# Optimization experiments

Hardware: AMD Instinct MI355X
Metric: run time of the kernel (lower is better)

Reference implementation:

```python
import jax, jax.numpy as jnp
import numpy as np

N_HEAD = 16


def setup_inputs() -> dict:
    key = jax.random.key(0)
    ks = jax.random.split(key, 7)
    b, lq, lv = 2, 2048, 2048
    q_dim = k_dim = v_dim = 1024
    s = 0.02
    return {
        "q": jax.random.normal(ks[0], (b, lq, q_dim), jnp.float32),
        "k": jax.random.normal(ks[1], (b, lv, k_dim), jnp.float32),
        "v": jax.random.normal(ks[2], (b, lv, v_dim), jnp.float32),
        "Wq": jax.random.normal(ks[3], (k_dim, q_dim), jnp.float32) * s,  # torch Linear: [out, in]
        "Wk": jax.random.normal(ks[4], (k_dim, k_dim), jnp.float32) * s,
        "Wv": jax.random.normal(ks[5], (v_dim, v_dim), jnp.float32) * s,
        "Wo": jax.random.normal(ks[6], (v_dim, v_dim), jnp.float32) * s,
    }


def reference(q, k, v, Wq, Wk, Wv, Wo):
    b, lq, _ = q.shape
    lv = k.shape[1]
    qp = q @ Wq.T  # [b, lq, k_dim]
    kp = k @ Wk.T  # [b, lv, k_dim]
    vp = v @ Wv.T  # [b, lv, v_dim]
    # split heads: [b, h, l, d]
    qh = qp.reshape(b, lq, N_HEAD, -1).transpose(0, 2, 1, 3)
    kh = kp.reshape(b, lv, N_HEAD, -1).transpose(0, 2, 1, 3)
    vh = vp.reshape(b, lv, N_HEAD, -1).transpose(0, 2, 1, 3)
    d = qh.shape[-1]
    scores = jnp.einsum("bhqd,bhkd->bhqk", qh, kh) / jnp.sqrt(jnp.float32(d))
    p = jax.nn.softmax(scores, axis=-1)
    attn = jnp.einsum("bhqk,bhkd->bhqd", p, vh)
    attn = attn.transpose(0, 2, 1, 3).reshape(b, lq, -1)  # [b, lq, v_dim]
    return attn @ Wo.T
```

## Files before the change

kernel.cpp:

```cpp
#include <hip/hip_runtime.h>
#include <hip/hip_bf16.h>
#include <stdint.h>

typedef __attribute__((ext_vector_type(8))) short bf16x8;
typedef __attribute__((ext_vector_type(4))) float f32x4;
typedef __attribute__((ext_vector_type(16))) float f32x16;
typedef __attribute__((ext_vector_type(2))) uint32_t u32x2;
typedef __attribute__((ext_vector_type(4))) uint32_t u32x4;

#define LQ 2048
#define CDIM 1024
#define NTOK 4096
#define WELEM 1048576
#define TELEM 4194304

__device__ __forceinline__ short f2bf(float f) {
  union { float f; uint32_t u; } v; v.f = f;
  uint32_t r = v.u + 0x7fffu + ((v.u >> 16) & 1u);
  return (short)(r >> 16);
}

__device__ __forceinline__ uint32_t cvt_pk_bf16(float a, float b) {
  uint32_t r;
  asm("v_cvt_pk_bf16_f32 %0, %1, %2" : "=v"(r) : "v"(a), "v"(b));
  return r;
}

__device__ __forceinline__ float fexp2(float x) {
  float r;
  asm("v_exp_f32 %0, %1" : "=v"(r) : "v"(x));
  return r;
}

__device__ __forceinline__ int swz(int row, int col) {
  return (row << 6) + (col ^ ((row & 7) << 3));
}

__device__ __forceinline__ void gl_lds16(const void* g, void* lds) {
  __builtin_amdgcn_global_load_lds(
      (const __attribute__((address_space(1))) void*)g,
      (__attribute__((address_space(3))) void*)lds, 16, 0, 0);
}

__device__ __forceinline__ void plswap(uint32_t& a, uint32_t& b) {
  asm volatile("s_nop 1\n\tv_permlane32_swap_b32 %0, %1\n\ts_nop 1" : "+v"(a), "+v"(b));
}

__device__ __forceinline__ bf16x8 mkfrag(const float* p) {
  uint32_t w0 = cvt_pk_bf16(p[0], p[1]);
  uint32_t w1 = cvt_pk_bf16(p[2], p[3]);
  uint32_t w2 = cvt_pk_bf16(p[4], p[5]);
  uint32_t w3 = cvt_pk_bf16(p[6], p[7]);
  plswap(w0, w2);
  plswap(w1, w3);
  union { u32x4 u; bf16x8 h; } cv;
  cv.u = u32x4{w0, w1, w2, w3};
  return cv.h;
}

__global__ __launch_bounds__(256) void convall_kernel(const float* __restrict__ wq, const float* __restrict__ wk,
                                                      const float* __restrict__ wv, const float* __restrict__ wo,
                                                      const float* __restrict__ q, const float* __restrict__ k,
                                                      const float* __restrict__ v,
                                                      short* __restrict__ wbf, short* __restrict__ qb,
                                                      short* __restrict__ kb, short* __restrict__ vb) {
  const int NG = (4 * WELEM + 3 * TELEM) / 8;
  for (int i = blockIdx.x * 256 + threadIdx.x; i < NG; i += gridDim.x * 256) {
    int e = i * 8;
    const float* s;
    short* d;
    if (e < 4 * WELEM) {
      int seg = e >> 20;
      int off = e & (WELEM - 1);
      s = (seg == 0 ? wq : seg == 1 ? wk : seg == 2 ? wv : wo) + off;
      d = wbf + e;
    } else {
      int j = e - 4 * WELEM;
      int which = j >> 22;
      int off = j & (TELEM - 1);
      s = (which == 0 ? q : which == 1 ? k : v) + off;
      d = (which == 0 ? qb : which == 1 ? kb : vb) + off;
    }
    f32x4 x0 = *(const f32x4*)(s);
    f32x4 x1 = *(const f32x4*)(s + 4);
    u32x4 r = { cvt_pk_bf16(x0[0], x0[1]), cvt_pk_bf16(x0[2], x0[3]),
                cvt_pk_bf16(x1[0], x1[1]), cvt_pk_bf16(x1[2], x1[3]) };
    *(u32x4*)(d) = r;
  }
}

template<int CMODE, int BN>
__device__ __forceinline__ void gemm_bb(short* __restrict__ AbP, short* __restrict__ BbP,
                                        const short* __restrict__ Ap, const short* __restrict__ Bp,
                                        void* Cp, int m0, int n0, int K, int ldc)
{
  const int t = threadIdx.x;
  const int lane = t & 63;
  const int wid = t >> 6;
  const int l15 = lane & 15, l4 = lane >> 4;
  constexpr int NI = (BN == 128) ? 4 : 2;
  const int wr = (BN == 128) ? (wid >> 1) * 64 : wid * 32;
  const int wc = (BN == 128) ? (wid & 1) * 64 : 0;

  f32x4 acc[NI][4];
#pragma unroll
  for (int i = 0; i < NI; ++i)
#pragma unroll
    for (int j = 0; j < 4; ++j) acc[i][j] = f32x4{0.f, 0.f, 0.f, 0.f};

  const int grow = lane >> 3;
  const int gcol = ((lane & 7) ^ grow) * 8;
  constexpr int AI = 4, BI = BN / 32;
  const short* asrc = Ap + (size_t)(m0 + wid * 32 + grow) * K + gcol;
  const short* bsrc = Bp + (size_t)(n0 + wid * (BN / 4) + grow) * K + gcol;

#pragma unroll
  for (int c = 0; c < AI; ++c) gl_lds16(asrc + (size_t)c * 8 * K, AbP + (wid * AI + c) * 512);
#pragma unroll
  for (int c = 0; c < BI; ++c) gl_lds16(bsrc + (size_t)c * 8 * K, BbP + (wid * BI + c) * 512);

  const int NT = K / 64;
  for (int kt = 0; kt < NT; ++kt) {
    const int cur = kt & 1;
    if (kt + 1 < NT) {
      const short* a2 = asrc + (size_t)(kt + 1) * 64;
      const short* b2 = bsrc + (size_t)(kt + 1) * 64;
#pragma unroll
      for (int c = 0; c < AI; ++c)
        gl_lds16(a2 + (size_t)c * 8 * K, AbP + (cur ^ 1) * 8192 + (wid * AI + c) * 512);
#pragma unroll
      for (int c = 0; c < BI; ++c)
        gl_lds16(b2 + (size_t)c * 8 * K, BbP + (cur ^ 1) * (BN * 64) + (wid * BI + c) * 512);
      if constexpr (BN == 128) asm volatile("s_waitcnt vmcnt(8)" ::: "memory");
      else                     asm volatile("s_waitcnt vmcnt(6)" ::: "memory");
    } else {
      asm volatile("s_waitcnt vmcnt(0)" ::: "memory");
    }
    __builtin_amdgcn_sched_barrier(0);
    __builtin_amdgcn_s_barrier();
    __builtin_amdgcn_sched_barrier(0);

    const short* Al = AbP + cur * 8192;
    const short* Bl = BbP + cur * (BN * 64);
#pragma unroll
    for (int kh = 0; kh < 2; ++kh) {
      bf16x8 af[NI], bfr[4];
#pragma unroll
      for (int i = 0; i < NI; ++i)
        af[i] = *(const bf16x8*)&Al[swz(wr + i * 16 + l15, kh * 32 + l4 * 8)];
#pragma unroll
      for (int j = 0; j < 4; ++j)
        bfr[j] = *(const bf16x8*)&Bl[swz(wc + j * 16 + l15, kh * 32 + l4 * 8)];
      __builtin_amdgcn_s_setprio(1);
#pragma unroll
      for (int i = 0; i < NI; ++i)
#pragma unroll
        for (int j = 0; j < 4; ++j)
          acc[i][j] = __builtin_amdgcn_mfma_f32_16x16x32_bf16(af[i], bfr[j], acc[i][j], 0, 0, 0);
      __builtin_amdgcn_s_setprio(0);
    }
    __builtin_amdgcn_sched_barrier(0);
    __builtin_amdgcn_s_barrier();
  }

#pragma unroll
  for (int i = 0; i < NI; ++i)
#pragma unroll
    for (int j = 0; j < 4; ++j) {
      if constexpr (CMODE == 2) {
        int rr0 = m0 + wr + i * 16 + l4 * 4;
        int cc = n0 + wc + j * 16 + l15;
        size_t idx = ((size_t)(((rr0 >> 11) << 4) + (cc >> 6)) * 64 + (cc & 63)) * 2048 + (rr0 & 2047);
        u32x2 w = { cvt_pk_bf16(acc[i][j][0], acc[i][j][1]),
                    cvt_pk_bf16(acc[i][j][2], acc[i][j][3]) };
        *(u32x2*)((short*)Cp + idx) = w;
      } else {
#pragma unroll
        for (int r = 0; r < 4; ++r) {
          int rr = m0 + wr + i * 16 + l4 * 4 + r;
          int cc = n0 + wc + j * 16 + l15;
          if constexpr (CMODE == 0) ((float*)Cp)[(size_t)rr * ldc + cc] = acc[i][j][r];
          else                      ((short*)Cp)[(size_t)rr * ldc + cc] = f2bf(acc[i][j][r]);
        }
      }
    }
}

__global__ __launch_bounds__(256) void proj_kernel(const short* __restrict__ qb, const short* __restrict__ kb,
                                                   const short* __restrict__ vb, const short* __restrict__ wbf,
                                                   short* __restrict__ qp, short* __restrict__ kp,
                                                   short* __restrict__ vpt)
{
  __shared__ alignas(16) short Ab[2 * 8192];
  __shared__ alignas(16) short Bb[2 * 8192];
  int nb = blockIdx.y;
  int sel = nb >> 3;
  int n0 = (nb & 7) * 128;
  int m0 = blockIdx.x * 128;
  if (sel == 2) {
    gemm_bb<2, 128>(Ab, Bb, vb, wbf + (size_t)2 * WELEM, vpt, m0, n0, CDIM, CDIM);
  } else {
    const short* A = sel == 0 ? qb : kb;
    const short* B = wbf + (size_t)sel * WELEM;
    short* C = sel == 0 ? qp : kp;
    gemm_bb<1, 128>(Ab, Bb, A, B, C, m0, n0, CDIM, CDIM);
  }
}

__global__ __launch_bounds__(256) void out_kernel(const short* __restrict__ at, const short* __restrict__ wo,
                                                  float* __restrict__ out)
{
  __shared__ alignas(16) short Ab[2 * 8192];
  __shared__ alignas(16) short Bb[2 * 4096];
  gemm_bb<0, 64>(Ab, Bb, at, wo, out, blockIdx.x * 128, blockIdx.y * 64, CDIM, CDIM);
}

__global__ __launch_bounds__(256) void attn_kernel(const short* __restrict__ kp, const short* __restrict__ vpt,
                                                   short* __restrict__ qp)
{
  __shared__ alignas(16) short Kbuf[2][64 * 64];
  __shared__ alignas(16) short Vbuf[2][64 * 64];

  const int bh = blockIdx.x;
  const int b = bh >> 4, h = bh & 15;
  const int q0 = blockIdx.y * 128;
  const int t = threadIdx.x, lane = t & 63, wid = t >> 6;
  const int l31 = lane & 31, hi = lane >> 5;
  const size_t base = (size_t)b * LQ * CDIM + (size_t)h * 64;
  const int qw = q0 + wid * 32;

  bf16x8 qf[4];
  {
    const short* qrow = qp + base + (size_t)(qw + l31) * CDIM + hi * 8;
    qf[0] = *(const bf16x8*)(qrow);
    qf[1] = *(const bf16x8*)(qrow + 16);
    qf[2] = *(const bf16x8*)(qrow + 32);
    qf[3] = *(const bf16x8*)(qrow + 48);
  }

  bf16x8 ones;
#pragma unroll
  for (int j = 0; j < 8; ++j) ones[j] = (short)0x3F80;

  f32x16 o0, o1, lacc;
#pragma unroll
  for (int r = 0; r < 16; ++r) { o0[r] = 0.f; o1[r] = 0.f; lacc[r] = 0.f; }

  const int grp = lane >> 3;
  const int chk = ((lane & 7) ^ grp) * 8;
  const short* ksrc = kp + base + (size_t)(wid * 16 + grp) * CDIM + chk;
  const short* vsrc = vpt + (size_t)bh * 64 * 2048 + (size_t)(wid * 16 + grp) * 2048 + chk;

  const float SC2 = 0.18033688011112042f;
  const int NT = LQ / 64;

  gl_lds16(ksrc, &Kbuf[0][(wid * 16) * 64]);
  gl_lds16(ksrc + (size_t)8 * CDIM, &Kbuf[0][(wid * 16 + 8) * 64]);
  gl_lds16(vsrc, &Vbuf[0][(wid * 16) * 64]);
  gl_lds16(vsrc + (size_t)8 * 2048, &Vbuf[0][(wid * 16 + 8) * 64]);

  for (int kt = 0; kt < NT; ++kt) {
    const int cur = kt & 1;
    if (kt + 1 < NT) {
      const short* ks = ksrc + (size_t)(kt + 1) * 64 * CDIM;
      const short* vs = vsrc + (size_t)(kt + 1) * 64;
      gl_lds16(ks, &Kbuf[cur ^ 1][(wid * 16) * 64]);
      gl_lds16(ks + (size_t)8 * CDIM, &Kbuf[cur ^ 1][(wid * 16 + 8) * 64]);
      gl_lds16(vs, &Vbuf[cur ^ 1][(wid * 16) * 64]);
      gl_lds16(vs + (size_t)8 * 2048, &Vbuf[cur ^ 1][(wid * 16 + 8) * 64]);
      asm volatile("s_waitcnt vmcnt(4)" ::: "memory");
    } else {
      asm volatile("s_waitcnt vmcnt(0)" ::: "memory");
    }
    __builtin_amdgcn_sched_barrier(0);
    __builtin_amdgcn_s_barrier();
    __builtin_amdgcn_sched_barrier(0);

    const short* Klds = Kbuf[cur];
    const short* Vt = Vbuf[cur];

    f32x16 c0, c1;
#pragma unroll
    for (int r = 0; r < 16; ++r) { c0[r] = 0.f; c1[r] = 0.f; }
    __builtin_amdgcn_s_setprio(1);
#pragma unroll
    for (int ds = 0; ds < 4; ++ds) {
      bf16x8 ka = *(const bf16x8*)&Klds[swz(l31, ds * 16 + hi * 8)];
      bf16x8 kb = *(const bf16x8*)&Klds[swz(32 + l31, ds * 16 + hi * 8)];
      c0 = __builtin_amdgcn_mfma_f32_32x32x16_bf16(ka, qf[ds], c0, 0, 0, 0);
      c1 = __builtin_amdgcn_mfma_f32_32x32x16_bf16(kb, qf[ds], c1, 0, 0, 0);
    }
    __builtin_amdgcn_s_setprio(0);

    float pr0[16], pr1[16];
#pragma unroll
    for (int r = 0; r < 16; ++r) {
      pr0[r] = fexp2(c0[r] * SC2);
      pr1[r] = fexp2(c1[r] * SC2);
    }

    bf16x8 pa0 = mkfrag(pr0);
    bf16x8 pa1 = mkfrag(pr0 + 8);
    bf16x8 pa2 = mkfrag(pr1);
    bf16x8 pa3 = mkfrag(pr1 + 8);

    __builtin_amdgcn_s_setprio(1);
#pragma unroll
    for (int ks = 0; ks < 4; ++ks) {
      bf16x8 pa = ks == 0 ? pa0 : ks == 1 ? pa1 : ks == 2 ? pa2 : pa3;
      bf16x8 v0 = *(const bf16x8*)&Vt[swz(l31, ks * 16 + hi * 8)];
      bf16x8 v1 = *(const bf16x8*)&Vt[swz(32 + l31, ks * 16 + hi * 8)];
      o0 = __builtin_amdgcn_mfma_f32_32x32x16_bf16(v0, pa, o0, 0, 0, 0);
      o1 = __builtin_amdgcn_mfma_f32_32x32x16_bf16(v1, pa, o1, 0, 0, 0);
      lacc = __builtin_amdgcn_mfma_f32_32x32x16_bf16(ones, pa, lacc, 0, 0, 0);
    }
    __builtin_amdgcn_s_setprio(0);
    __builtin_amdgcn_sched_barrier(0);
    __builtin_amdgcn_s_barrier();
  }

  float inv = 1.0f / lacc[0];
  short* orow = qp + base + (size_t)(qw + l31) * CDIM;
#pragma unroll
  for (int rq = 0; rq < 4; ++rq) {
    u32x2 w;
    w[0] = cvt_pk_bf16(o0[rq * 4 + 0] * inv, o0[rq * 4 + 1] * inv);
    w[1] = cvt_pk_bf16(o0[rq * 4 + 2] * inv, o0[rq * 4 + 3] * inv);
    *(u32x2*)(orow + rq * 8 + hi * 4) = w;
    w[0] = cvt_pk_bf16(o1[rq * 4 + 0] * inv, o1[rq * 4 + 1] * inv);
    w[1] = cvt_pk_bf16(o1[rq * 4 + 2] * inv, o1[rq * 4 + 3] * inv);
    *(u32x2*)(orow + 32 + rq * 8 + hi * 4) = w;
  }
}

extern "C" void kernel_launch(void* const* d_in, const int* in_sizes, int n_in,
                              void* d_out, int out_size, void* d_ws, size_t ws_size,
                              hipStream_t stream) {
  const float* q  = (const float*)d_in[0];
  const float* k  = (const float*)d_in[1];
  const float* v  = (const float*)d_in[2];
  const float* Wq = (const float*)d_in[3];
  const float* Wk = (const float*)d_in[4];
  const float* Wv = (const float*)d_in[5];
  const float* Wo = (const float*)d_in[6];
  float* out = (float*)d_out;

  short* wbf = (short*)d_ws;
  short* vb  = wbf + (size_t)4 * WELEM;
  short* qp  = vb + (size_t)TELEM;
  short* kp  = qp + (size_t)TELEM;
  short* vpt = kp + (size_t)TELEM;
  short* qb = (short*)d_out;
  short* kb = qb + (size_t)TELEM;

  convall_kernel<<<2048, 256, 0, stream>>>(Wq, Wk, Wv, Wo, q, k, v, wbf, qb, kb, vb);
  proj_kernel<<<dim3(32, 24), 256, 0, stream>>>(qb, kb, vb, wbf, qp, kp, vpt);
  attn_kernel<<<dim3(32, 16), 256, 0, stream>>>(kp, vpt, qp);
  out_kernel<<<dim3(32, 16), 256, 0, stream>>>(qp, wbf + (size_t)3 * WELEM, out);
}
```

Measured before the change: 120.1 us.

## Fuse activation fp32-to-bf16 conversion into projection GEMM and split MFMA accumulators

After: 188.5 us. +56.9%, slower.

```diff
diff --git a/kernel.cpp b/kernel.cpp
--- a/kernel.cpp
+++ b/kernel.cpp
@@ -58,41 +58,27 @@
   return cv.h;
 }
 
-__global__ __launch_bounds__(256) void convall_kernel(const float* __restrict__ wq, const float* __restrict__ wk,
-                                                      const float* __restrict__ wv, const float* __restrict__ wo,
-                                                      const float* __restrict__ q, const float* __restrict__ k,
-                                                      const float* __restrict__ v,
-                                                      short* __restrict__ wbf, short* __restrict__ qb,
-                                                      short* __restrict__ kb, short* __restrict__ vb) {
-  const int NG = (4 * WELEM + 3 * TELEM) / 8;
+__global__ __launch_bounds__(256) void convw_kernel(const float* __restrict__ wq, const float* __restrict__ wk,
+                                                    const float* __restrict__ wv, const float* __restrict__ wo,
+                                                    short* __restrict__ wbf) {
+  const int NG = (4 * WELEM) / 8;
   for (int i = blockIdx.x * 256 + threadIdx.x; i < NG; i += gridDim.x * 256) {
     int e = i * 8;
-    const float* s;
-    short* d;
-    if (e < 4 * WELEM) {
-      int seg = e >> 20;
-      int off = e & (WELEM - 1);
-      s = (seg == 0 ? wq : seg == 1 ? wk : seg == 2 ? wv : wo) + off;
-      d = wbf + e;
-    } else {
-      int j = e - 4 * WELEM;
-      int which = j >> 22;
-      int off = j & (TELEM - 1);
-      s = (which == 0 ? q : which == 1 ? k : v) + off;
-      d = (which == 0 ? qb : which == 1 ? kb : vb) + off;
-    }
+    int seg = e >> 20;
+    int off = e & (WELEM - 1);
+    const float* s = (seg == 0 ? wq : seg == 1 ? wk : seg == 2 ? wv : wo) + off;
     f32x4 x0 = *(const f32x4*)(s);
     f32x4 x1 = *(const f32x4*)(s + 4);
     u32x4 r = { cvt_pk_bf16(x0[0], x0[1]), cvt_pk_bf16(x0[2], x0[3]),
                 cvt_pk_bf16(x1[0], x1[1]), cvt_pk_bf16(x1[2], x1[3]) };
-    *(u32x4*)(d) = r;
-  }
-}
-
-template<int CMODE, int BN>
+    *(u32x4*)(wbf + e) = r;
+  }
+}
+
+template<int CMODE, int BN, bool AF32>
 __device__ __forceinline__ void gemm_bb(short* __restrict__ AbP, short* __restrict__ BbP,
-                                        const short* __restrict__ Ap, const short* __restrict__ Bp,
-                                        void* Cp, int m0, int n0, int K, int ldc)
+                                        const void* Ap, const short* __restrict__ Bp,
+                                        void* Cp, int m0, int n0, int K, int ldc, float cscale)
 {
   const int t = threadIdx.x;
   const int lane = t & 63;
@@ -111,37 +97,72 @@
   const int grow = lane >> 3;
   const int gcol = ((lane & 7) ^ grow) * 8;
   constexpr int AI = 4, BI = BN / 32;
-  const short* asrc = Ap + (size_t)(m0 + wid * 32 + grow) * K + gcol;
   const short* bsrc = Bp + (size_t)(n0 + wid * (BN / 4) + grow) * K + gcol;
-
-#pragma unroll
-  for (int c = 0; c < AI; ++c) gl_lds16(asrc + (size_t)c * 8 * K, AbP + (wid * AI + c) * 512);
+  const short* asrcb = (const short*)Ap + (size_t)(m0 + wid * 32 + grow) * K + gcol;
+  const int arow = t >> 1, acol = (t & 1) * 32;
+  const float* asrcf = (const float*)Ap + (size_t)(m0 + arow) * K + acol;
+  f32x4 va[8];
+
 #pragma unroll
   for (int c = 0; c < BI; ++c) gl_lds16(bsrc + (size_t)c * 8 * K, BbP + (wid * BI + c) * 512);
+  if constexpr (AF32) {
+#pragma unroll
+    for (int c = 0; c < 8; ++c) va[c] = *(const f32x4*)(asrcf + c * 4);
+  } else {
+#pragma unroll
+    for (int c = 0; c < AI; ++c) gl_lds16(asrcb + (size_t)c * 8 * K, AbP + (wid * AI + c) * 512);
+  }
 
   const int NT = K / 64;
   for (int kt = 0; kt < NT; ++kt) {
     const int cur = kt & 1;
-    if (kt + 1 < NT) {
-      const short* a2 = asrc + (size_t)(kt + 1) * 64;
-      const short* b2 = bsrc + (size_t)(kt + 1) * 64;
-#pragma unroll
-      for (int c = 0; c < AI; ++c)
-        gl_lds16(a2 + (size_t)c * 8 * K, AbP + (cur ^ 1) * 8192 + (wid * AI + c) * 512);
-#pragma unroll
-      for (int c = 0; c < BI; ++c)
-        gl_lds16(b2 + (size_t)c * 8 * K, BbP + (cur ^ 1) * (BN * 64) + (wid * BI + c) * 512);
-      if constexpr (BN == 128) asm volatile("s_waitcnt vmcnt(8)" ::: "memory");
-      else                     asm volatile("s_waitcnt vmcnt(6)" ::: "memory");
+    short* Al = AbP + cur * 8192;
+    const short* Bl = BbP + cur * (BN * 64);
+
+    if constexpr (AF32) {
+      if (kt + 1 < NT) {
+        const short* b2 = bsrc + (size_t)(kt + 1) * 64;
+#pragma unroll
+        for (int c = 0; c < BI; ++c)
+          gl_lds16(b2 + (size_t)c * 8 * K, BbP + (cur ^ 1) * (BN * 64) + (wid * BI + c) * 512);
+        asm volatile("s_waitcnt vmcnt(4)" ::: "memory");
+      } else {
+        asm volatile("s_waitcnt vmcnt(0)" ::: "memory");
+      }
+#pragma unroll
+      for (int c2 = 0; c2 < 4; ++c2) {
+        u32x4 w = { cvt_pk_bf16(va[2 * c2][0], va[2 * c2][1]),
+                    cvt_pk_bf16(va[2 * c2][2], va[2 * c2][3]),
+                    cvt_pk_bf16(va[2 * c2 + 1][0], va[2 * c2 + 1][1]),
+                    cvt_pk_bf16(va[2 * c2 + 1][2], va[2 * c2 + 1][3]) };
+        *(u32x4*)&Al[swz(arow, acol + c2 * 8)] = w;
+      }
+      if (kt + 1 < NT) {
+        const float* a2 = asrcf + (size_t)(kt + 1) * 64;
+#pragma unroll
+        for (int c = 0; c < 8; ++c) va[c] = *(const f32x4*)(a2 + c * 4);
+      }
+      asm volatile("s_waitcnt lgkmcnt(0)" ::: "memory");
     } else {
-      asm volatile("s_waitcnt vmcnt(0)" ::: "memory");
+      if (kt + 1 < NT) {
+        const short* a2 = asrcb + (size_t)(kt + 1) * 64;
+        const short* b2 = bsrc + (size_t)(kt + 1) * 64;
+#pragma unroll
+        for (int c = 0; c < AI; ++c)
+          gl_lds16(a2 + (size_t)c * 8 * K, AbP + (cur ^ 1) * 8192 + (wid * AI + c) * 512);
+#pragma unroll
+        for (int c = 0; c < BI; ++c)
+          gl_lds16(b2 + (size_t)c * 8 * K, BbP + (cur ^ 1) * (BN * 64) + (wid * BI + c) * 512);
+        if constexpr (BN == 128) asm volatile("s_waitcnt vmcnt(8)" ::: "memory");
+        else                     asm volatile("s_waitcnt vmcnt(6)" ::: "memory");
+      } else {
+        asm volatile("s_waitcnt vmcnt(0)" ::: "memory");
+      }
     }
     __builtin_amdgcn_sched_barrier(0);
     __builtin_amdgcn_s_barrier();
     __builtin_amdgcn_sched_barrier(0);
 
-    const short* Al = AbP + cur * 8192;
-    const short* Bl = BbP + cur * (BN * 64);
 #pragma unroll
     for (int kh = 0; kh < 2; ++kh) {
       bf16x8 af[NI], bfr[4];
@@ -180,31 +201,30 @@
           int rr = m0 + wr + i * 16 + l4 * 4 + r;
           int cc = n0 + wc + j * 16 + l15;
           if constexpr (CMODE == 0) ((float*)Cp)[(size_t)rr * ldc + cc] = acc[i][j][r];
-          else                      ((short*)Cp)[(size_t)rr * ldc + cc] = f2bf(acc[i][j][r]);
+          else                      ((short*)Cp)[(size_t)rr * ldc + cc] = f2bf(acc[i][j][r] * cscale);
         }
       }
     }
 }
 
-__global__ __launch_bounds__(256) void proj_kernel(const short* __restrict__ qb, const short* __restrict__ kb,
-                                                   const short* __restrict__ vb, const short* __restrict__ wbf,
+__global__ __launch_bounds__(256) void proj_kernel(const float* __restrict__ q, const float* __restrict__ k,
+                                                   const float* __restrict__ v, const short* __restrict__ wbf,
                                                    short* __restrict__ qp, short* __restrict__ kp,
                                                    short* __restrict__ vpt)
 {
   __shared__ alignas(16) short Ab[2 * 8192];
   __shared__ alignas(16) short Bb[2 * 8192];
+  const float SC2 = 0.18033688011112042f;
   int nb = blockIdx.y;
   int sel = nb >> 3;
   int n0 = (nb & 7) * 128;
   int m0 = blockIdx.x * 128;
-  if (sel == 2) {
-    gemm_bb<2, 128>(Ab, Bb, vb, wbf + (size_t)2 * WELEM, vpt, m0, n0, CDIM, CDIM);
-  } else {
-    const short* A = sel == 0 ? qb : kb;
-    const short* B = wbf + (size_t)sel * WELEM;
-    short* C = sel == 0 ? qp : kp;
-    gemm_bb<1, 128>(Ab, Bb, A, B, C, m0, n0, CDIM, CDIM);
-  }
+  if (sel == 0)
+    gemm_bb<1, 128, true>(Ab, Bb, q, wbf, qp, m0, n0, CDIM, CDIM, SC2);
+  else if (sel == 1)
+    gemm_bb<1, 128, true>(Ab, Bb, k, wbf + (size_t)WELEM, kp, m0, n0, CDIM, CDIM, 1.0f);
+  else
+    gemm_bb<2, 128, true>(Ab, Bb, v, wbf + (size_t)2 * WELEM, vpt, m0, n0, CDIM, CDIM, 1.0f);
 }
 
 __global__ __launch_bounds__(256) void out_kernel(const short* __restrict__ at, const short* __restrict__ wo,
@@ -212,7 +232,7 @@
 {
   __shared__ alignas(16) short Ab[2 * 8192];
   __shared__ alignas(16) short Bb[2 * 4096];
-  gemm_bb<0, 64>(Ab, Bb, at, wo, out, blockIdx.x * 128, blockIdx.y * 64, CDIM, CDIM);
+  gemm_bb<0, 64, false>(Ab, Bb, at, wo, out, blockIdx.x * 128, blockIdx.y * 64, CDIM, CDIM, 1.0f);
 }
 
 __global__ __launch_bounds__(256) void attn_kernel(const short* __restrict__ kp, const short* __restrict__ vpt,
@@ -242,16 +262,17 @@
 #pragma unroll
   for (int j = 0; j < 8; ++j) ones[j] = (short)0x3F80;
 
-  f32x16 o0, o1, lacc;
-#pragma unroll
-  for (int r = 0; r < 16; ++r) { o0[r] = 0.f; o1[r] = 0.f; lacc[r] = 0.f; }
+  f32x16 o0a, o0b, o1a, o1b, lacca, laccb;
+#pragma unroll
+  for (int r = 0; r < 16; ++r) {
+    o0a[r] = 0.f; o0b[r] = 0.f; o1a[r] = 0.f; o1b[r] = 0.f; lacca[r] = 0.f; laccb[r] = 0.f;
+  }
 
   const int grp = lane >> 3;
   const int chk = ((lane & 7) ^ grp) * 8;
   const short* ksrc = kp + base + (size_t)(wid * 16 + grp) * CDIM + chk;
   const short* vsrc = vpt + (size_t)bh * 64 * 2048 + (size_t)(wid * 16 + grp) * 2048 + chk;
 
-  const float SC2 = 0.18033688011112042f;
   const int NT = LQ / 64;
 
   gl_lds16(ksrc, &Kbuf[0][(wid * 16) * 64]);
@@ -279,24 +300,29 @@
     const short* Klds = Kbuf[cur];
     const short* Vt = Vbuf[cur];
 
-    f32x16 c0, c1;
-#pragma unroll
-    for (int r = 0; r < 16; ++r) { c0[r] = 0.f; c1[r] = 0.f; }
+    f32x16 c0a, c0b, c1a, c1b;
+#pragma unroll
+    for (int r = 0; r < 16; ++r) { c0a[r] = 0.f; c0b[r] = 0.f; c1a[r] = 0.f; c1b[r] = 0.f; }
     __builtin_amdgcn_s_setprio(1);
 #pragma unroll
     for (int ds = 0; ds < 4; ++ds) {
       bf16x8 ka = *(const bf16x8*)&Klds[swz(l31, ds * 16 + hi * 8)];
       bf16x8 kb = *(const bf16x8*)&Klds[swz(32 + l31, ds * 16 + hi * 8)];
-      c0 = __builtin_amdgcn_mfma_f32_32x32x16_bf16(ka, qf[ds], c0, 0, 0, 0);
-      c1 = __builtin_amdgcn_mfma_f32_32x32x16_bf16(kb, qf[ds], c1, 0, 0, 0);
+      if (ds & 1) {
+        c0b = __builtin_amdgcn_mfma_f32_32x32x16_bf16(ka, qf[ds], c0b, 0, 0, 0);
+        c1b = __builtin_amdgcn_mfma_f32_32x32x16_bf16(kb, qf[ds], c1b, 0, 0, 0);
+      } else {
+        c0a = __builtin_amdgcn_mfma_f32_32x32x16_bf16(ka, qf[ds], c0a, 0, 0, 0);
+        c1a = __builtin_amdgcn_mfma_f32_32x32x16_bf16(kb, qf[ds], c1a, 0, 0, 0);
+      }
     }
     __builtin_amdgcn_s_setprio(0);
 
     float pr0[16], pr1[16];
 #pragma unroll
     for (int r = 0; r < 16; ++r) {
-      pr0[r] = fexp2(c0[r] * SC2);
-      pr1[r] = fexp2(c1[r] * SC2);
+      pr0[r] = fexp2(c0a[r] + c0b[r]);
+      pr1[r] = fexp2(c1a[r] + c1b[r]);
     }
 
     bf16x8 pa0 = mkfrag(pr0);
@@ -310,25 +336,35 @@
       bf16x8 pa = ks == 0 ? pa0 : ks == 1 ? pa1 : ks == 2 ? pa2 : pa3;
       bf16x8 v0 = *(const bf16x8*)&Vt[swz(l31, ks * 16 + hi * 8)];
       bf16x8 v1 = *(const bf16x8*)&Vt[swz(32 + l31, ks * 16 + hi * 8)];
-      o0 = __builtin_amdgcn_mfma_f32_32x32x16_bf16(v0, pa, o0, 0, 0, 0);
-      o1 = __builtin_amdgcn_mfma_f32_32x32x16_bf16(v1, pa, o1, 0, 0, 0);
-      lacc = __builtin_amdgcn_mfma_f32_32x32x16_bf16(ones, pa, lacc, 0, 0, 0);
+      if (ks < 2) {
+        o0a = __builtin_amdgcn_mfma_f32_32x32x16_bf16(v0, pa, o0a, 0, 0, 0);
+        o1a = __builtin_amdgcn_mfma_f32_32x32x16_bf16(v1, pa, o1a, 0, 0, 0);
+        lacca = __builtin_amdgcn_mfma_f32_32x32x16_bf16(ones, pa, lacca, 0, 0, 0);
+      } else {
+        o0b = __builtin_amdgcn_mfma_f32_32x32x16_bf16(v0, pa, o0b, 0, 0, 0);
+        o1b = __builtin_amdgcn_mfma_f32_32x32x16_bf16(v1, pa, o1b, 0, 0, 0);
+        laccb = __builtin_amdgcn_mfma_f32_32x32x16_bf16(ones, pa, laccb, 0, 0, 0);
+      }
     }
     __builtin_amdgcn_s_setprio(0);
     __builtin_amdgcn_sched_barrier(0);
     __builtin_amdgcn_s_barrier();
   }
 
-  float inv = 1.0f / lacc[0];
+  float inv = 1.0f / (lacca[0] + laccb[0]);
   short* orow = qp + base + (size_t)(qw + l31) * CDIM;
 #pragma unroll
   for (int rq = 0; rq < 4; ++rq) {
     u32x2 w;
-    w[0] = cvt_pk_bf16(o0[rq * 4 + 0] * inv, o0[rq * 4 + 1] * inv);
-    w[1] = cvt_pk_bf16(o0[rq * 4 + 2] * inv, o0[rq * 4 + 3] * inv);
+    w[0] = cvt_pk_bf16((o0a[rq * 4 + 0] + o0b[rq * 4 + 0]) * inv,
+                       (o0a[rq * 4 + 1] + o0b[rq * 4 + 1]) * inv);
+    w[1] = cvt_pk_bf16((o0a[rq * 4 + 2] + o0b[rq * 4 + 2]) * inv,
+                       (o0a[rq * 4 + 3] + o0b[rq * 4 + 3]) * inv);
     *(u32x2*)(orow + rq * 8 + hi * 4) = w;
-    w[0] = cvt_pk_bf16(o1[rq * 4 + 0] * inv, o1[rq * 4 + 1] * inv);
-    w[1] = cvt_pk_bf16(o1[rq * 4 + 2] * inv, o1[rq * 4 + 3] * inv);
+    w[0] = cvt_pk_bf16((o1a[rq * 4 + 0] + o1b[rq * 4 + 0]) * inv,
+                       (o1a[rq * 4 + 1] + o1b[rq * 4 + 1]) * inv);
+    w[1] = cvt_pk_bf16((o1a[rq * 4 + 2] + o1b[rq * 4 + 2]) * inv,
+                       (o1a[rq * 4 + 3] + o1b[rq * 4 + 3]) * inv);
     *(u32x2*)(orow + 32 + rq * 8 + hi * 4) = w;
   }
 }
@@ -346,15 +382,12 @@
   float* out = (float*)d_out;
 
   short* wbf = (short*)d_ws;
-  short* vb  = wbf + (size_t)4 * WELEM;
-  short* qp  = vb + (size_t)TELEM;
+  short* qp  = wbf + (size_t)4 * WELEM;
   short* kp  = qp + (size_t)TELEM;
   short* vpt = kp + (size_t)TELEM;
-  short* qb = (short*)d_out;
-  short* kb = qb + (size_t)TELEM;
-
-  convall_kernel<<<2048, 256, 0, stream>>>(Wq, Wk, Wv, Wo, q, k, v, wbf, qb, kb, vb);
-  proj_kernel<<<dim3(32, 24), 256, 0, stream>>>(qb, kb, vb, wbf, qp, kp, vpt);
+
+  convw_kernel<<<512, 256, 0, stream>>>(Wq, Wk, Wv, Wo, wbf);
+  proj_kernel<<<dim3(32, 24), 256, 0, stream>>>(q, k, v, wbf, qp, kp, vpt);
   attn_kernel<<<dim3(32, 16), 256, 0, stream>>>(kp, vpt, qp);
   out_kernel<<<dim3(32, 16), 256, 0, stream>>>(qp, wbf + (size_t)3 * WELEM, out);
 }
```

## Split attention over two KV halves and combine partial outputs in separate kernel

Applied to the files above, without the earlier changes.

New measurement: 128.2 us. +6.7%, slower.

```diff
diff --git a/kernel.cpp b/kernel.cpp
--- a/kernel.cpp
+++ b/kernel.cpp
@@ -18,6 +18,11 @@
   union { float f; uint32_t u; } v; v.f = f;
   uint32_t r = v.u + 0x7fffu + ((v.u >> 16) & 1u);
   return (short)(r >> 16);
+}
+
+__device__ __forceinline__ float bf2f(short s) {
+  union { uint32_t u; float f; } v; v.u = ((uint32_t)(uint16_t)s) << 16;
+  return v.f;
 }
 
 __device__ __forceinline__ uint32_t cvt_pk_bf16(float a, float b) {
@@ -92,7 +97,7 @@
 template<int CMODE, int BN>
 __device__ __forceinline__ void gemm_bb(short* __restrict__ AbP, short* __restrict__ BbP,
                                         const short* __restrict__ Ap, const short* __restrict__ Bp,
-                                        void* Cp, int m0, int n0, int K, int ldc)
+                                        void* Cp, int m0, int n0, int K, int ldc, float cscale)
 {
   const int t = threadIdx.x;
   const int lane = t & 63;
@@ -180,7 +185,7 @@
           int rr = m0 + wr + i * 16 + l4 * 4 + r;
           int cc = n0 + wc + j * 16 + l15;
           if constexpr (CMODE == 0) ((float*)Cp)[(size_t)rr * ldc + cc] = acc[i][j][r];
-          else                      ((short*)Cp)[(size_t)rr * ldc + cc] = f2bf(acc[i][j][r]);
+          else                      ((short*)Cp)[(size_t)rr * ldc + cc] = f2bf(acc[i][j][r] * cscale);
         }
       }
     }
@@ -193,18 +198,17 @@
 {
   __shared__ alignas(16) short Ab[2 * 8192];
   __shared__ alignas(16) short Bb[2 * 8192];
+  const float SC2 = 0.18033688011112042f;
   int nb = blockIdx.y;
   int sel = nb >> 3;
   int n0 = (nb & 7) * 128;
   int m0 = blockIdx.x * 128;
-  if (sel == 2) {
-    gemm_bb<2, 128>(Ab, Bb, vb, wbf + (size_t)2 * WELEM, vpt, m0, n0, CDIM, CDIM);
-  } else {
-    const short* A = sel == 0 ? qb : kb;
-    const short* B = wbf + (size_t)sel * WELEM;
-    short* C = sel == 0 ? qp : kp;
-    gemm_bb<1, 128>(Ab, Bb, A, B, C, m0, n0, CDIM, CDIM);
-  }
+  if (sel == 0)
+    gemm_bb<1, 128>(Ab, Bb, qb, wbf, qp, m0, n0, CDIM, CDIM, SC2);
+  else if (sel == 1)
+    gemm_bb<1, 128>(Ab, Bb, kb, wbf + (size_t)WELEM, kp, m0, n0, CDIM, CDIM, 1.0f);
+  else
+    gemm_bb<2, 128>(Ab, Bb, vb, wbf + (size_t)2 * WELEM, vpt, m0, n0, CDIM, CDIM, 1.0f);
 }
 
 __global__ __launch_bounds__(256) void out_kernel(const short* __restrict__ at, const short* __restrict__ wo,
@@ -212,11 +216,13 @@
 {
   __shared__ alignas(16) short Ab[2 * 8192];
   __shared__ alignas(16) short Bb[2 * 4096];
-  gemm_bb<0, 64>(Ab, Bb, at, wo, out, blockIdx.x * 128, blockIdx.y * 64, CDIM, CDIM);
+  gemm_bb<0, 64>(Ab, Bb, at, wo, out, blockIdx.x * 128, blockIdx.y * 64, CDIM, CDIM, 1.0f);
 }
 
 __global__ __launch_bounds__(256) void attn_kernel(const short* __restrict__ kp, const short* __restrict__ vpt,
-                                                   short* __restrict__ qp)
+                                                   const short* __restrict__ qp,
+                                                   short* __restrict__ op0, short* __restrict__ op1,
+                                                   float* __restrict__ laccbuf)
 {
   __shared__ alignas(16) short Kbuf[2][64 * 64];
   __shared__ alignas(16) short Vbuf[2][64 * 64];
@@ -224,6 +230,7 @@
   const int bh = blockIdx.x;
   const int b = bh >> 4, h = bh & 15;
   const int q0 = blockIdx.y * 128;
+  const int kvh = blockIdx.z;
   const int t = threadIdx.x, lane = t & 63, wid = t >> 6;
   const int l31 = lane & 31, hi = lane >> 5;
   const size_t base = (size_t)b * LQ * CDIM + (size_t)h * 64;
@@ -248,11 +255,11 @@
 
   const int grp = lane >> 3;
   const int chk = ((lane & 7) ^ grp) * 8;
-  const short* ksrc = kp + base + (size_t)(wid * 16 + grp) * CDIM + chk;
-  const short* vsrc = vpt + (size_t)bh * 64 * 2048 + (size_t)(wid * 16 + grp) * 2048 + chk;
-
-  const float SC2 = 0.18033688011112042f;
-  const int NT = LQ / 64;
+  const short* ksrc = kp + base + (size_t)(kvh * 1024 + wid * 16 + grp) * CDIM + chk;
+  const short* vsrc = vpt + (size_t)bh * 64 * 2048 + (size_t)(wid * 16 + grp) * 2048
+                          + kvh * 1024 + chk;
+
+  const int NT = 1024 / 64;
 
   gl_lds16(ksrc, &Kbuf[0][(wid * 16) * 64]);
   gl_lds16(ksrc + (size_t)8 * CDIM, &Kbuf[0][(wid * 16 + 8) * 64]);
@@ -295,8 +302,8 @@
     float pr0[16], pr1[16];
 #pragma unroll
     for (int r = 0; r < 16; ++r) {
-      pr0[r] = fexp2(c0[r] * SC2);
-      pr1[r] = fexp2(c1[r] * SC2);
+      pr0[r] = fexp2(c0[r]);
+      pr1[r] = fexp2(c1[r]);
     }
 
     bf16x8 pa0 = mkfrag(pr0);
@@ -319,18 +326,43 @@
     __builtin_amdgcn_s_barrier();
   }
 
-  float inv = 1.0f / lacc[0];
-  short* orow = qp + base + (size_t)(qw + l31) * CDIM;
+  short* opart = kvh == 0 ? op0 : op1;
+  short* orow = opart + base + (size_t)(qw + l31) * CDIM;
 #pragma unroll
   for (int rq = 0; rq < 4; ++rq) {
     u32x2 w;
-    w[0] = cvt_pk_bf16(o0[rq * 4 + 0] * inv, o0[rq * 4 + 1] * inv);
-    w[1] = cvt_pk_bf16(o0[rq * 4 + 2] * inv, o0[rq * 4 + 3] * inv);
+    w[0] = cvt_pk_bf16(o0[rq * 4 + 0], o0[rq * 4 + 1]);
+    w[1] = cvt_pk_bf16(o0[rq * 4 + 2], o0[rq * 4 + 3]);
     *(u32x2*)(orow + rq * 8 + hi * 4) = w;
-    w[0] = cvt_pk_bf16(o1[rq * 4 + 0] * inv, o1[rq * 4 + 1] * inv);
-    w[1] = cvt_pk_bf16(o1[rq * 4 + 2] * inv, o1[rq * 4 + 3] * inv);
+    w[0] = cvt_pk_bf16(o1[rq * 4 + 0], o1[rq * 4 + 1]);
+    w[1] = cvt_pk_bf16(o1[rq * 4 + 2], o1[rq * 4 + 3]);
     *(u32x2*)(orow + 32 + rq * 8 + hi * 4) = w;
   }
+  if (hi == 0)
+    laccbuf[kvh * 65536 + bh * 2048 + qw + l31] = lacc[0];
+}
+
+__global__ __launch_bounds__(256) void combine_kernel(const short* __restrict__ op0,
+                                                      const short* __restrict__ op1,
+                                                      const float* __restrict__ laccbuf,
+                                                      short* __restrict__ qp)
+{
+  int i = (blockIdx.x * 256 + threadIdx.x) * 8;
+  bf16x8 pa = *(const bf16x8*)(op0 + i);
+  bf16x8 pb = *(const bf16x8*)(op1 + i);
+  int q = (i >> 10) & 2047;
+  int h = (i >> 6) & 15;
+  int b = i >> 21;
+  int li = (b * 16 + h) * 2048 + q;
+  float inv = 1.0f / (laccbuf[li] + laccbuf[65536 + li]);
+  u32x4 r;
+#pragma unroll
+  for (int j = 0; j < 4; ++j) {
+    float lo = (bf2f(pa[2 * j]) + bf2f(pb[2 * j])) * inv;
+    float hi2 = (bf2f(pa[2 * j + 1]) + bf2f(pb[2 * j + 1])) * inv;
+    r[j] = cvt_pk_bf16(lo, hi2);
+  }
+  *(u32x4*)(qp + i) = r;
 }
 
 extern "C" void kernel_launch(void* const* d_in, const int* in_sizes, int n_in,
@@ -350,11 +382,15 @@
   short* qp  = vb + (size_t)TELEM;
   short* kp  = qp + (size_t)TELEM;
   short* vpt = kp + (size_t)TELEM;
+  short* op1 = vpt + (size_t)TELEM;
+  float* laccbuf = (float*)(op1 + (size_t)TELEM);
   short* qb = (short*)d_out;
   short* kb = qb + (size_t)TELEM;
+  short* op0 = (short*)d_out;
 
   convall_kernel<<<2048, 256, 0, stream>>>(Wq, Wk, Wv, Wo, q, k, v, wbf, qb, kb, vb);
   proj_kernel<<<dim3(32, 24), 256, 0, stream>>>(qb, kb, vb, wbf, qp, kp, vpt);
-  attn_kernel<<<dim3(32, 16), 256, 0, stream>>>(kp, vpt, qp);
+  attn_kernel<<<dim3(32, 16, 2), 256, 0, stream>>>(kp, vpt, qp, op0, op1, laccbuf);
+  combine_kernel<<<2048, 256, 0, stream>>>(op0, op1, laccbuf, qp);
   out_kernel<<<dim3(32, 16), 256, 0, stream>>>(qp, wbf + (size_t)3 * WELEM, out);
 }
```
